# Optimization experiments

Measured on AMD Instinct MI355X. Metric: run time of the kernel, lower is better.

Reference implementation:

```python
import jax, jax.numpy as jnp
import numpy as np

IN_FEATURES = 512
OUT_FEATURES = 128
KERNEL_DIMS = 16
BATCH = 256


def setup_inputs() -> dict:
    key = jax.random.key(0)
    kx, kT = jax.random.split(key)
    x = jax.random.normal(kx, (BATCH, IN_FEATURES), dtype=jnp.float32)
    # nn.init.normal_(T, 0, 1)
    T = jax.random.normal(kT, (IN_FEATURES, OUT_FEATURES, KERNEL_DIMS), dtype=jnp.float32)
    return {"x": x, "T": T}


def reference(x, T):
    B = x.shape[0]
    in_f, out_f, kd = T.shape
    # matrices: [B, out_features, kernel_dims]
    matrices = (x @ T.reshape(in_f, out_f * kd)).reshape(B, out_f, kd)
    # pairwise L1 distance over kernel dim: [B, B, out_features]
    # diff[a, b] = matrices[b] - matrices[a] (abs makes it symmetric)
    norm = jnp.abs(matrices[None, :, :, :] - matrices[:, None, :, :]).sum(axis=3)
    expnorm = jnp.exp(-norm)  # [B, B, out_features]
    o_b = expnorm.sum(axis=0)  # mean=False -> keep self-term (=1)
    return jnp.concatenate([x, o_b], axis=1)  # [B, in_features + out_features]
```

## Files before the change

### kernel.cpp

```cpp
#include <hip/hip_runtime.h>
#include <hip/hip_fp16.h>
#include <stdint.h>

#define NB 256
#define NK 512
#define NO 128
#define NC 2048
#define OUTW 640

typedef __attribute__((ext_vector_type(8))) short bf16x8;
typedef __attribute__((ext_vector_type(4))) float f32x4;
typedef __attribute__((ext_vector_type(4))) unsigned int u32x4;
typedef __attribute__((ext_vector_type(2))) unsigned int u32x2;

__device__ __forceinline__ unsigned int pk(float lo, float hi) {
  return __builtin_amdgcn_perm(__builtin_bit_cast(unsigned int, hi),
                               __builtin_bit_cast(unsigned int, lo), 0x07060302u);
}

__global__ __launch_bounds__(256) void k_gemm(const float* __restrict__ x,
                                              const float* __restrict__ T,
                                              float* __restrict__ out,
                                              __half* __restrict__ mt) {
  __shared__ unsigned short lds[2][12288];
  const int tid = threadIdx.x;
  const int bn = blockIdx.x * 64;
  const int bm = blockIdx.y * 32;
  const int lane = tid & 63, wid = tid >> 6;
  const int wr = wid >> 1, wc = wid & 1;

  {
    const int bid = blockIdx.y * 32 + blockIdx.x;
    if (tid < 128) {
      int idx = bid * 128 + tid;
      int row = idx >> 7, c4 = (idx & 127) * 4;
      *(f32x4*)(out + (size_t)row * OUTW + c4) = *(const f32x4*)(x + (size_t)row * NK + c4);
    }
  }

  int arow[2], akg[2], bkb[2], bcb[2];
#pragma unroll
  for (int s = 0; s < 2; ++s) { int idx = tid + s * 256; arow[s] = idx >> 4; akg[s] = idx & 15; }
#pragma unroll
  for (int s = 0; s < 2; ++s) { int idx = tid + s * 256; bkb[s] = idx >> 4; bcb[s] = idx & 15; }

  f32x4 raf[2][2], rbf[2][4];
  auto loadG = [&](int t) {
#pragma unroll
    for (int s = 0; s < 2; ++s) {
      const float* p = x + (size_t)(bm + arow[s]) * NK + t * 128 + akg[s] * 8;
      raf[s][0] = *(const f32x4*)p;
      raf[s][1] = *(const f32x4*)(p + 4);
    }
#pragma unroll
    for (int s = 0; s < 2; ++s)
#pragma unroll
      for (int j = 0; j < 4; ++j)
        rbf[s][j] = *(const f32x4*)(T + (size_t)(t * 128 + bkb[s] * 4 + j) * NC + bn + bcb[s] * 4);
  };
  auto writeS = [&](int b) {
#pragma unroll
    for (int s = 0; s < 2; ++s) {
      u32x4 w;
      w[0] = pk(raf[s][0][0], raf[s][0][1]);
      w[1] = pk(raf[s][0][2], raf[s][0][3]);
      w[2] = pk(raf[s][1][0], raf[s][1][1]);
      w[3] = pk(raf[s][1][2], raf[s][1][3]);
      *(u32x4*)(&lds[b][arow[s] * 128 + ((akg[s] ^ (arow[s] & 7)) << 3)]) = w;
    }
#pragma unroll
    for (int s = 0; s < 2; ++s) {
      const int kb = bkb[s], kg = kb >> 1, k0l = (kb & 1) * 4;
#pragma unroll
      for (int c = 0; c < 4; ++c) {
        u32x2 w;
        w[0] = pk(rbf[s][0][c], rbf[s][1][c]);
        w[1] = pk(rbf[s][2][c], rbf[s][3][c]);
        int bc = bcb[s] * 4 + c;
        *(u32x2*)(&lds[b][4096 + bc * 128 + ((kg ^ (bc & 7)) << 3) + k0l]) = w;
      }
    }
  };

  f32x4 acc[2] = {};
  const int rowA  = wr * 16 + (lane & 15);
  const int colB0 = wc * 32 + (lane & 15);

  loadG(0); writeS(0); __syncthreads();
#pragma unroll
  for (int t = 0; t < 4; ++t) {
    if (t < 3) loadG(t + 1);
    const int b = t & 1;
#pragma unroll
    for (int ks = 0; ks < 4; ++ks) {
      int kg = ks * 4 + (lane >> 4);
      bf16x8 af = *(const bf16x8*)(&lds[b][rowA * 128 + ((kg ^ (rowA & 7)) << 3)]);
#pragma unroll
      for (int ct = 0; ct < 2; ++ct) {
        int col = colB0 + ct * 16;
        bf16x8 bv = *(const bf16x8*)(&lds[b][4096 + col * 128 + ((kg ^ (col & 7)) << 3)]);
        acc[ct] = __builtin_amdgcn_mfma_f32_16x16x32_bf16(af, bv, acc[ct], 0, 0, 0);
      }
    }
    if (t < 3) writeS((t + 1) & 1);
    __syncthreads();
  }

#pragma unroll
  for (int ct = 0; ct < 2; ++ct) {
    int colg = bn + wc * 32 + ct * 16 + (lane & 15);
    int o = colg >> 4, kd = colg & 15;
    int rbase = bm + wr * 16 + (lane >> 4) * 4;
#pragma unroll
    for (int j = 0; j < 4; ++j)
      mt[(size_t)o * 4096 + (size_t)(rbase + j) * 16 + kd] = __float2half(acc[ct][j]);
  }
}

__global__ __launch_bounds__(256, 4) void k_pair(const __half* __restrict__ mt,
                                                 float* __restrict__ out) {
  __shared__ unsigned char S[8192];
  __shared__ float red[32][33];
  const int tid = threadIdx.x, bid = blockIdx.x;
  const int o = bid >> 3, bq = bid & 7;
  const __half* __restrict__ mo = mt + (size_t)o * 4096;

#pragma unroll
  for (int s = 0; s < 2; ++s) {
    int idx = tid + s * 256;
    int row = idx >> 1, h = idx & 1;
    u32x4 v = ((const u32x4*)mo)[idx];
    *(u32x4*)(&S[((row * 32) ^ (((row >> 2) & 3) << 5)) + h * 16]) = v;
  }
  __syncthreads();

  const int bg = tid & 7, aq = tid >> 3;
  const int wv = tid >> 6, aqr = aq & 7;
  const int r0 = bq * 32 + bg * 4;

  __half2 br[4][8];
#pragma unroll
  for (int r = 0; r < 4; ++r) {
    const __half2* p = (const __half2*)&S[((r0 + r) * 32) ^ ((((r0 + r) >> 2) & 3) << 5)];
#pragma unroll
    for (int i = 0; i < 8; ++i) br[r][i] = p[i];
  }

  float acc[4] = {0.f, 0.f, 0.f, 0.f};
#pragma unroll 2
  for (int it = 0; it < 8; ++it) {
    const int a = it * 32 + wv * 8 + aqr;
    const __half2* pa = (const __half2*)&S[(a * 32) ^ (((a >> 2) & 3) << 5)];
    __half2 ra[8];
#pragma unroll
    for (int i = 0; i < 8; ++i) ra[i] = pa[i];
#pragma unroll
    for (int r = 0; r < 4; ++r) {
      __half2 s2 = __habs2(__hsub2(ra[0], br[r][0]));
#pragma unroll
      for (int i = 1; i < 8; ++i)
        s2 = __hadd2(s2, __habs2(__hsub2(ra[i], br[r][i])));
      float n = __low2float(s2) + __high2float(s2);
      acc[r] += __expf(-n);
    }
  }
#pragma unroll
  for (int r = 0; r < 4; ++r) red[aq][bg * 4 + r] = acc[r];
  __syncthreads();
  if (tid < 32) {
    float s = 0.f;
#pragma unroll
    for (int q = 0; q < 32; ++q) s += red[q][tid];
    out[(size_t)(bq * 32 + tid) * OUTW + NK + o] = s;
  }
}

extern "C" void kernel_launch(void* const* d_in, const int* in_sizes, int n_in,
                              void* d_out, int out_size, void* d_ws, size_t ws_size,
                              hipStream_t stream) {
  const float* x = (const float*)d_in[0];
  const float* T = (const float*)d_in[1];
  float* out = (float*)d_out;
  __half* mt = (__half*)d_ws;

  k_gemm<<<dim3(32, 8), 256, 0, stream>>>(x, T, out, mt);
  k_pair<<<1024, 256, 0, stream>>>(mt, out);
}
```

Measured before the change: 20.62 us.

## Fuse GEMM and pairwise L1-exp kernels into one per-output-feature kernel

Merges the projection GEMM and the pairwise distance kernel into a single launch. Each of 256 blocks (two per output feature) recomputes the full 256x16 projection slice for its feature in LDS and then computes half of the pairwise sums, so the fp16 intermediate no longer goes through global memory and the second launch is gone. In exchange, each block redundantly streams all of x (256x512) and the GEMM work is doubled across the two halves. The GEMM now runs with a single LDS buffer and two barriers per k-step instead of double buffering.

```diff
diff --git a/kernel.cpp b/kernel.cpp
--- a/kernel.cpp
+++ b/kernel.cpp
@@ -17,140 +17,110 @@
   return __builtin_amdgcn_perm(__builtin_bit_cast(unsigned int, hi),
                                __builtin_bit_cast(unsigned int, lo), 0x07060302u);
 }
+__device__ __forceinline__ int swzrow(int r) {
+  return (r * 32) ^ (((r >> 2) & 3) << 5);
+}
 
-__global__ __launch_bounds__(256) void k_gemm(const float* __restrict__ x,
-                                              const float* __restrict__ T,
-                                              float* __restrict__ out,
-                                              __half* __restrict__ mt) {
-  __shared__ unsigned short lds[2][12288];
-  const int tid = threadIdx.x;
-  const int bn = blockIdx.x * 64;
-  const int bm = blockIdx.y * 32;
-  const int lane = tid & 63, wid = tid >> 6;
-  const int wr = wid >> 1, wc = wid & 1;
+__global__ __launch_bounds__(512, 2) void k_one(const float* __restrict__ x,
+                                                const float* __restrict__ T,
+                                                float* __restrict__ out) {
+  __shared__ alignas(16) unsigned char smem[34816];
+  unsigned short* lds = (unsigned short*)smem;
+  const int tid = threadIdx.x, bid = blockIdx.x;
+  const int o = bid >> 1, hf = bid & 1;
 
-  {
-    const int bid = blockIdx.y * 32 + blockIdx.x;
-    if (tid < 128) {
-      int idx = bid * 128 + tid;
-      int row = idx >> 7, c4 = (idx & 127) * 4;
-      *(f32x4*)(out + (size_t)row * OUTW + c4) = *(const f32x4*)(x + (size_t)row * NK + c4);
-    }
+  if (tid < 128) {
+    int idx = bid * 128 + tid;
+    int row = idx >> 7, c4 = (idx & 127) * 4;
+    *(f32x4*)(out + (size_t)row * OUTW + c4) = *(const f32x4*)(x + (size_t)row * NK + c4);
   }
 
-  int arow[2], akg[2], bkb[2], bcb[2];
+  int arow[4], akg[4];
 #pragma unroll
-  for (int s = 0; s < 2; ++s) { int idx = tid + s * 256; arow[s] = idx >> 4; akg[s] = idx & 15; }
-#pragma unroll
-  for (int s = 0; s < 2; ++s) { int idx = tid + s * 256; bkb[s] = idx >> 4; bcb[s] = idx & 15; }
+  for (int s = 0; s < 4; ++s) { int idx = tid + s * 512; arow[s] = idx >> 3; akg[s] = idx & 7; }
+  const int bkq = tid >> 2, bcq = tid & 3;
 
-  f32x4 raf[2][2], rbf[2][4];
+  f32x4 raf[4][2], rbf[4];
   auto loadG = [&](int t) {
 #pragma unroll
-    for (int s = 0; s < 2; ++s) {
-      const float* p = x + (size_t)(bm + arow[s]) * NK + t * 128 + akg[s] * 8;
+    for (int s = 0; s < 4; ++s) {
+      const float* p = x + (size_t)arow[s] * NK + t * 64 + akg[s] * 8;
       raf[s][0] = *(const f32x4*)p;
       raf[s][1] = *(const f32x4*)(p + 4);
     }
-#pragma unroll
-    for (int s = 0; s < 2; ++s)
+    if (tid < 64) {
 #pragma unroll
       for (int j = 0; j < 4; ++j)
-        rbf[s][j] = *(const f32x4*)(T + (size_t)(t * 128 + bkb[s] * 4 + j) * NC + bn + bcb[s] * 4);
+        rbf[j] = *(const f32x4*)(T + (size_t)(t * 64 + bkq * 4 + j) * NC + o * 16 + bcq * 4);
+    }
   };
-  auto writeS = [&](int b) {
+  auto writeS = [&]() {
 #pragma unroll
-    for (int s = 0; s < 2; ++s) {
+    for (int s = 0; s < 4; ++s) {
       u32x4 w;
-      w[0] = pk(raf[s][0][0], raf[s][0][1]);
-      w[1] = pk(raf[s][0][2], raf[s][0][3]);
-      w[2] = pk(raf[s][1][0], raf[s][1][1]);
-      w[3] = pk(raf[s][1][2], raf[s][1][3]);
-      *(u32x4*)(&lds[b][arow[s] * 128 + ((akg[s] ^ (arow[s] & 7)) << 3)]) = w;
+      w[0] = pk(raf[s][0][0], raf[s][0][1]); w[1] = pk(raf[s][0][2], raf[s][0][3]);
+      w[2] = pk(raf[s][1][0], raf[s][1][1]); w[3] = pk(raf[s][1][2], raf[s][1][3]);
+      *(u32x4*)(&lds[arow[s] * 64 + ((akg[s] ^ (arow[s] & 7)) << 3)]) = w;
     }
-#pragma unroll
-    for (int s = 0; s < 2; ++s) {
-      const int kb = bkb[s], kg = kb >> 1, k0l = (kb & 1) * 4;
+    if (tid < 64) {
 #pragma unroll
       for (int c = 0; c < 4; ++c) {
-        u32x2 w;
-        w[0] = pk(rbf[s][0][c], rbf[s][1][c]);
-        w[1] = pk(rbf[s][2][c], rbf[s][3][c]);
-        int bc = bcb[s] * 4 + c;
-        *(u32x2*)(&lds[b][4096 + bc * 128 + ((kg ^ (bc & 7)) << 3) + k0l]) = w;
+        int cc = bcq * 4 + c;
+        u32x2 w2;
+        w2[0] = pk(rbf[0][c], rbf[1][c]);
+        w2[1] = pk(rbf[2][c], rbf[3][c]);
+        *(u32x2*)(&lds[16384 + cc * 64 + (((bkq >> 1) ^ (cc & 7)) << 3) + ((bkq & 1) << 2)]) = w2;
       }
     }
   };
 
+  const int lane = tid & 63, wv = tid >> 6;
   f32x4 acc[2] = {};
-  const int rowA  = wr * 16 + (lane & 15);
-  const int colB0 = wc * 32 + (lane & 15);
-
-  loadG(0); writeS(0); __syncthreads();
+  loadG(0); writeS(); __syncthreads();
 #pragma unroll
-  for (int t = 0; t < 4; ++t) {
-    if (t < 3) loadG(t + 1);
-    const int b = t & 1;
+  for (int t = 0; t < 8; ++t) {
+    if (t < 7) loadG(t + 1);
 #pragma unroll
-    for (int ks = 0; ks < 4; ++ks) {
+    for (int ks = 0; ks < 2; ++ks) {
       int kg = ks * 4 + (lane >> 4);
-      bf16x8 af = *(const bf16x8*)(&lds[b][rowA * 128 + ((kg ^ (rowA & 7)) << 3)]);
+      bf16x8 bv = *(const bf16x8*)(&lds[16384 + (lane & 15) * 64 + ((kg ^ (lane & 7)) << 3)]);
 #pragma unroll
-      for (int ct = 0; ct < 2; ++ct) {
-        int col = colB0 + ct * 16;
-        bf16x8 bv = *(const bf16x8*)(&lds[b][4096 + col * 128 + ((kg ^ (col & 7)) << 3)]);
-        acc[ct] = __builtin_amdgcn_mfma_f32_16x16x32_bf16(af, bv, acc[ct], 0, 0, 0);
+      for (int tl = 0; tl < 2; ++tl) {
+        int row = wv * 32 + tl * 16 + (lane & 15);
+        bf16x8 af = *(const bf16x8*)(&lds[row * 64 + ((kg ^ (row & 7)) << 3)]);
+        acc[tl] = __builtin_amdgcn_mfma_f32_16x16x32_bf16(af, bv, acc[tl], 0, 0, 0);
       }
     }
-    if (t < 3) writeS((t + 1) & 1);
     __syncthreads();
+    if (t < 7) { writeS(); __syncthreads(); }
   }
 
 #pragma unroll
-  for (int ct = 0; ct < 2; ++ct) {
-    int colg = bn + wc * 32 + ct * 16 + (lane & 15);
-    int o = colg >> 4, kd = colg & 15;
-    int rbase = bm + wr * 16 + (lane >> 4) * 4;
+  for (int tl = 0; tl < 2; ++tl) {
+    int c = lane & 15;
+    int rb = wv * 32 + tl * 16 + (lane >> 4) * 4;
 #pragma unroll
     for (int j = 0; j < 4; ++j)
-      mt[(size_t)o * 4096 + (size_t)(rbase + j) * 16 + kd] = __float2half(acc[ct][j]);
-  }
-}
-
-__global__ __launch_bounds__(256, 4) void k_pair(const __half* __restrict__ mt,
-                                                 float* __restrict__ out) {
-  __shared__ unsigned char S[8192];
-  __shared__ float red[32][33];
-  const int tid = threadIdx.x, bid = blockIdx.x;
-  const int o = bid >> 3, bq = bid & 7;
-  const __half* __restrict__ mo = mt + (size_t)o * 4096;
-
-#pragma unroll
-  for (int s = 0; s < 2; ++s) {
-    int idx = tid + s * 256;
-    int row = idx >> 1, h = idx & 1;
-    u32x4 v = ((const u32x4*)mo)[idx];
-    *(u32x4*)(&S[((row * 32) ^ (((row >> 2) & 3) << 5)) + h * 16]) = v;
+      *(__half*)(&smem[swzrow(rb + j) + c * 2]) = __float2half(acc[tl][j]);
   }
   __syncthreads();
 
-  const int bg = tid & 7, aq = tid >> 3;
-  const int wv = tid >> 6, aqr = aq & 7;
-  const int r0 = bq * 32 + bg * 4;
+  float* red = (float*)(smem + 8192);
+  const int bg = tid & 31, aq = tid >> 5;
+  const int r0 = hf * 128 + bg * 4;
 
   __half2 br[4][8];
 #pragma unroll
   for (int r = 0; r < 4; ++r) {
-    const __half2* p = (const __half2*)&S[((r0 + r) * 32) ^ ((((r0 + r) >> 2) & 3) << 5)];
+    const __half2* pb = (const __half2*)(&smem[swzrow(r0 + r)]);
 #pragma unroll
-    for (int i = 0; i < 8; ++i) br[r][i] = p[i];
+    for (int i = 0; i < 8; ++i) br[r][i] = pb[i];
   }
-
-  float acc[4] = {0.f, 0.f, 0.f, 0.f};
+  float acp[4] = {0.f, 0.f, 0.f, 0.f};
 #pragma unroll 2
-  for (int it = 0; it < 8; ++it) {
-    const int a = it * 32 + wv * 8 + aqr;
-    const __half2* pa = (const __half2*)&S[(a * 32) ^ (((a >> 2) & 3) << 5)];
+  for (int it = 0; it < 16; ++it) {
+    int a = aq * 16 + it;
+    const __half2* pa = (const __half2*)(&smem[swzrow(a)]);
     __half2 ra[8];
 #pragma unroll
     for (int i = 0; i < 8; ++i) ra[i] = pa[i];
@@ -161,17 +131,17 @@
       for (int i = 1; i < 8; ++i)
         s2 = __hadd2(s2, __habs2(__hsub2(ra[i], br[r][i])));
       float n = __low2float(s2) + __high2float(s2);
-      acc[r] += __expf(-n);
+      acp[r] += __expf(-n);
     }
   }
 #pragma unroll
-  for (int r = 0; r < 4; ++r) red[aq][bg * 4 + r] = acc[r];
+  for (int r = 0; r < 4; ++r) red[aq * 128 + bg * 4 + r] = acp[r];
   __syncthreads();
-  if (tid < 32) {
+  if (tid < 128) {
     float s = 0.f;
 #pragma unroll
-    for (int q = 0; q < 32; ++q) s += red[q][tid];
-    out[(size_t)(bq * 32 + tid) * OUTW + NK + o] = s;
+    for (int q = 0; q < 16; ++q) s += red[q * 128 + tid];
+    out[(size_t)(hf * 128 + tid) * OUTW + NK + o] = s;
   }
 }
 
@@ -181,8 +151,7 @@
   const float* x = (const float*)d_in[0];
   const float* T = (const float*)d_in[1];
   float* out = (float*)d_out;
-  __half* mt = (__half*)d_ws;
+  (void)d_ws; (void)ws_size;
 
-  k_gemm<<<dim3(32, 8), 256, 0, stream>>>(x, T, out, mt);
-  k_pair<<<1024, 256, 0, stream>>>(mt, out);
+  k_one<<<256, 512, 0, stream>>>(x, T, out);
 }
```

After: 21.27 us. 1.03x slower.

## Halve per-block tiles in both kernels and use shuffle reductions in pair kernel

Applied to the files above, without the earlier changes.

The GEMM kernel now uses 32-column tiles, launching twice as many blocks with one MFMA accumulator per wave. The pairwise kernel splits each output feature over 16 blocks of 16 rows instead of 8 blocks of 32. Each thread now handles 4 contiguous 'a' rows, and partial sums are reduced with wave shuffles plus a small 4x16 LDS array instead of a 32x33 one. The aim is more parallelism across CUs and less reduction overhead. The cost is that each block in both kernels does more redundant work: the pair kernel reloads the full 4096-element slice from global memory twice as often, and the GEMM kernel reloads the x tile twice as often.

```diff
diff --git a/kernel.cpp b/kernel.cpp
--- a/kernel.cpp
+++ b/kernel.cpp
@@ -17,34 +17,36 @@
   return __builtin_amdgcn_perm(__builtin_bit_cast(unsigned int, hi),
                                __builtin_bit_cast(unsigned int, lo), 0x07060302u);
 }
+__device__ __forceinline__ int swzrow(int r) {
+  return (r * 32) ^ (((r >> 2) & 3) << 5);
+}
 
-__global__ __launch_bounds__(256) void k_gemm(const float* __restrict__ x,
-                                              const float* __restrict__ T,
-                                              float* __restrict__ out,
-                                              __half* __restrict__ mt) {
-  __shared__ unsigned short lds[2][12288];
+__global__ __launch_bounds__(256, 2) void k_gemm(const float* __restrict__ x,
+                                                 const float* __restrict__ T,
+                                                 float* __restrict__ out,
+                                                 __half* __restrict__ mt) {
+  __shared__ unsigned short lds[2][8192];
   const int tid = threadIdx.x;
-  const int bn = blockIdx.x * 64;
+  const int bn = blockIdx.x * 32;
   const int bm = blockIdx.y * 32;
   const int lane = tid & 63, wid = tid >> 6;
   const int wr = wid >> 1, wc = wid & 1;
 
   {
-    const int bid = blockIdx.y * 32 + blockIdx.x;
-    if (tid < 128) {
-      int idx = bid * 128 + tid;
+    const int bid = blockIdx.y * 64 + blockIdx.x;
+    if (tid < 64) {
+      int idx = bid * 64 + tid;
       int row = idx >> 7, c4 = (idx & 127) * 4;
       *(f32x4*)(out + (size_t)row * OUTW + c4) = *(const f32x4*)(x + (size_t)row * NK + c4);
     }
   }
 
-  int arow[2], akg[2], bkb[2], bcb[2];
+  int arow[2], akg[2];
 #pragma unroll
   for (int s = 0; s < 2; ++s) { int idx = tid + s * 256; arow[s] = idx >> 4; akg[s] = idx & 15; }
-#pragma unroll
-  for (int s = 0; s < 2; ++s) { int idx = tid + s * 256; bkb[s] = idx >> 4; bcb[s] = idx & 15; }
+  const int bkb = tid >> 3, bcb = tid & 7;
 
-  f32x4 raf[2][2], rbf[2][4];
+  f32x4 raf[2][2], rbf[4];
   auto loadG = [&](int t) {
 #pragma unroll
     for (int s = 0; s < 2; ++s) {
@@ -53,10 +55,8 @@
       raf[s][1] = *(const f32x4*)(p + 4);
     }
 #pragma unroll
-    for (int s = 0; s < 2; ++s)
-#pragma unroll
-      for (int j = 0; j < 4; ++j)
-        rbf[s][j] = *(const f32x4*)(T + (size_t)(t * 128 + bkb[s] * 4 + j) * NC + bn + bcb[s] * 4);
+    for (int j = 0; j < 4; ++j)
+      rbf[j] = *(const f32x4*)(T + (size_t)(t * 128 + bkb * 4 + j) * NC + bn + bcb * 4);
   };
   auto writeS = [&](int b) {
 #pragma unroll
@@ -68,23 +68,22 @@
       w[3] = pk(raf[s][1][2], raf[s][1][3]);
       *(u32x4*)(&lds[b][arow[s] * 128 + ((akg[s] ^ (arow[s] & 7)) << 3)]) = w;
     }
-#pragma unroll
-    for (int s = 0; s < 2; ++s) {
-      const int kb = bkb[s], kg = kb >> 1, k0l = (kb & 1) * 4;
+    {
+      const int kg = bkb >> 1, k0l = (bkb & 1) * 4;
 #pragma unroll
       for (int c = 0; c < 4; ++c) {
-        u32x2 w;
-        w[0] = pk(rbf[s][0][c], rbf[s][1][c]);
-        w[1] = pk(rbf[s][2][c], rbf[s][3][c]);
-        int bc = bcb[s] * 4 + c;
-        *(u32x2*)(&lds[b][4096 + bc * 128 + ((kg ^ (bc & 7)) << 3) + k0l]) = w;
+        u32x2 w2;
+        w2[0] = pk(rbf[0][c], rbf[1][c]);
+        w2[1] = pk(rbf[2][c], rbf[3][c]);
+        int cc = bcb * 4 + c;
+        *(u32x2*)(&lds[b][4096 + cc * 128 + ((kg ^ (cc & 7)) << 3) + k0l]) = w2;
       }
     }
   };
 
-  f32x4 acc[2] = {};
-  const int rowA  = wr * 16 + (lane & 15);
-  const int colB0 = wc * 32 + (lane & 15);
+  f32x4 acc = {};
+  const int rowA = wr * 16 + (lane & 15);
+  const int colB = wc * 16 + (lane & 15);
 
   loadG(0); writeS(0); __syncthreads();
 #pragma unroll
@@ -95,34 +94,29 @@
     for (int ks = 0; ks < 4; ++ks) {
       int kg = ks * 4 + (lane >> 4);
       bf16x8 af = *(const bf16x8*)(&lds[b][rowA * 128 + ((kg ^ (rowA & 7)) << 3)]);
-#pragma unroll
-      for (int ct = 0; ct < 2; ++ct) {
-        int col = colB0 + ct * 16;
-        bf16x8 bv = *(const bf16x8*)(&lds[b][4096 + col * 128 + ((kg ^ (col & 7)) << 3)]);
-        acc[ct] = __builtin_amdgcn_mfma_f32_16x16x32_bf16(af, bv, acc[ct], 0, 0, 0);
-      }
+      bf16x8 bv = *(const bf16x8*)(&lds[b][4096 + colB * 128 + ((kg ^ (colB & 7)) << 3)]);
+      acc = __builtin_amdgcn_mfma_f32_16x16x32_bf16(af, bv, acc, 0, 0, 0);
     }
     if (t < 3) writeS((t + 1) & 1);
     __syncthreads();
   }
 
-#pragma unroll
-  for (int ct = 0; ct < 2; ++ct) {
-    int colg = bn + wc * 32 + ct * 16 + (lane & 15);
+  {
+    int colg = bn + wc * 16 + (lane & 15);
     int o = colg >> 4, kd = colg & 15;
     int rbase = bm + wr * 16 + (lane >> 4) * 4;
 #pragma unroll
     for (int j = 0; j < 4; ++j)
-      mt[(size_t)o * 4096 + (size_t)(rbase + j) * 16 + kd] = __float2half(acc[ct][j]);
+      mt[(size_t)o * 4096 + (size_t)(rbase + j) * 16 + kd] = __float2half(acc[j]);
   }
 }
 
-__global__ __launch_bounds__(256, 4) void k_pair(const __half* __restrict__ mt,
+__global__ __launch_bounds__(256, 6) void k_pair(const __half* __restrict__ mt,
                                                  float* __restrict__ out) {
   __shared__ unsigned char S[8192];
-  __shared__ float red[32][33];
+  __shared__ float red[4][16];
   const int tid = threadIdx.x, bid = blockIdx.x;
-  const int o = bid >> 3, bq = bid & 7;
+  const int o = bid >> 4, bs = bid & 15;
   const __half* __restrict__ mo = mt + (size_t)o * 4096;
 
 #pragma unroll
@@ -130,27 +124,27 @@
     int idx = tid + s * 256;
     int row = idx >> 1, h = idx & 1;
     u32x4 v = ((const u32x4*)mo)[idx];
-    *(u32x4*)(&S[((row * 32) ^ (((row >> 2) & 3) << 5)) + h * 16]) = v;
+    *(u32x4*)(&S[swzrow(row) + h * 16]) = v;
   }
   __syncthreads();
 
-  const int bg = tid & 7, aq = tid >> 3;
-  const int wv = tid >> 6, aqr = aq & 7;
-  const int r0 = bq * 32 + bg * 4;
+  const int bg = tid & 3, aq = tid >> 2;
+  const int lane = tid & 63, wv = tid >> 6;
+  const int r0 = bs * 16 + bg * 4;
 
   __half2 br[4][8];
 #pragma unroll
   for (int r = 0; r < 4; ++r) {
-    const __half2* p = (const __half2*)&S[((r0 + r) * 32) ^ ((((r0 + r) >> 2) & 3) << 5)];
+    const __half2* pb = (const __half2*)(&S[swzrow(r0 + r)]);
 #pragma unroll
-    for (int i = 0; i < 8; ++i) br[r][i] = p[i];
+    for (int i = 0; i < 8; ++i) br[r][i] = pb[i];
   }
 
   float acc[4] = {0.f, 0.f, 0.f, 0.f};
-#pragma unroll 2
-  for (int it = 0; it < 8; ++it) {
-    const int a = it * 32 + wv * 8 + aqr;
-    const __half2* pa = (const __half2*)&S[(a * 32) ^ (((a >> 2) & 3) << 5)];
+#pragma unroll
+  for (int it = 0; it < 4; ++it) {
+    const int a = aq * 4 + it;
+    const __half2* pa = (const __half2*)(&S[swzrow(a)]);
     __half2 ra[8];
 #pragma unroll
     for (int i = 0; i < 8; ++i) ra[i] = pa[i];
@@ -165,13 +159,20 @@
     }
   }
 #pragma unroll
-  for (int r = 0; r < 4; ++r) red[aq][bg * 4 + r] = acc[r];
+  for (int r = 0; r < 4; ++r) {
+    acc[r] += __shfl_down(acc[r], 4);
+    acc[r] += __shfl_down(acc[r], 8);
+    acc[r] += __shfl_down(acc[r], 16);
+    acc[r] += __shfl_down(acc[r], 32);
+  }
+  if (lane < 4) {
+#pragma unroll
+    for (int r = 0; r < 4; ++r) red[wv][lane * 4 + r] = acc[r];
+  }
   __syncthreads();
-  if (tid < 32) {
-    float s = 0.f;
-#pragma unroll
-    for (int q = 0; q < 32; ++q) s += red[q][tid];
-    out[(size_t)(bq * 32 + tid) * OUTW + NK + o] = s;
+  if (tid < 16) {
+    float s = red[0][tid] + red[1][tid] + red[2][tid] + red[3][tid];
+    out[(size_t)(bs * 16 + tid) * OUTW + NK + o] = s;
   }
 }
 
@@ -183,6 +184,6 @@
   float* out = (float*)d_out;
   __half* mt = (__half*)d_ws;
 
-  k_gemm<<<dim3(32, 8), 256, 0, stream>>>(x, T, out, mt);
-  k_pair<<<1024, 256, 0, stream>>>(mt, out);
+  k_gemm<<<dim3(64, 8), 256, 0, stream>>>(x, T, out, mt);
+  k_pair<<<2048, 256, 0, stream>>>(mt, out);
 }
```

Result: faster. 19.58 us (-5.1%).
